# Performance work log

Measured on AMD Instinct MI355X. Metric: run time of the kernel, lower is better.

Reference implementation:

```python
import jax, jax.numpy as jnp
import numpy as np


def setup_inputs() -> dict:
    key = jax.random.key(0)
    ks = jax.random.split(key, 8)
    N, C, T, V = 32, 64, 256, 25
    OUT, INTER, S = 64, 16, 3
    W_SCALE = 0.05  # keep complex softmax exp() well-conditioned
    return {
        "x_real": jax.random.normal(ks[0], (N, C, T, V), jnp.float32),
        "x_imag": jax.random.normal(ks[1], (N, C, T, V), jnp.float32),
        "A": jax.random.uniform(ks[2], (S, V, V), jnp.float32),
        "PA": jax.random.normal(ks[3], (S, V, V), jnp.float32) * 1e-3,
        "Wa": jax.random.normal(ks[4], (S, 2 * INTER, 2 * C), jnp.float32) * W_SCALE,
        "ba": jnp.zeros((S, 2 * INTER), jnp.float32),
        "Wb": jax.random.normal(ks[5], (S, 2 * INTER, 2 * C), jnp.float32) * W_SCALE,
        "bb": jnp.zeros((S, 2 * INTER), jnp.float32),
        "Wd": jax.random.normal(ks[6], (S, 2 * OUT, 2 * C), jnp.float32) * W_SCALE,
        "bd": jnp.zeros((S, 2 * OUT), jnp.float32),
        "bn_weight": jnp.ones((OUT,), jnp.float32),
        "bn_bias": jnp.zeros((OUT,), jnp.float32),
    }


def _cconv1x1(z, W, b):
    # C_Conv2d with k=1: 1x1 conv over concat(real, imag) channels.
    zc = jnp.concatenate([z.real, z.imag], axis=1)          # [N, 2*Cin, T, V]
    o = jnp.einsum("oc,nctv->notv", W, zc) + b[None, :, None, None]
    h = W.shape[0] // 2
    return jax.lax.complex(o[:, :h], o[:, h:])              # [N, Cout, T, V] complex


def _forward(x_real, x_imag, A, PA, Wa, ba, Wb, bb, Wd, bd, bn_weight, bn_bias):
    x = jax.lax.complex(x_real, x_imag)                     # [N, C, T, V]
    N, C, T, V = x.shape
    inter = Wa.shape[1] // 2
    Afull = A + PA                                          # [3, V, V] real
    X2 = x.reshape(N, C * T, V)
    y = None
    for i in range(A.shape[0]):
        A1 = _cconv1x1(x, Wa[i], ba[i])                     # [N, inter, T, V]
        A1 = A1.transpose(0, 3, 1, 2).reshape(N, V, inter * T)
        A2 = _cconv1x1(x, Wb[i], bb[i]).reshape(N, inter * T, V)
        S = jnp.matmul(A1, A2) / (inter * T)                # [N, V, V] complex
        # complex softmax over dim=1 (no max-subtraction, faithful to C_softmax)
        ez = jnp.exp(S)
        S = ez / jnp.sum(ez, axis=1, keepdims=True)
        S = S + Afull[i]
        z = jnp.matmul(X2, S).reshape(N, C, T, V)
        z = _cconv1x1(z, Wd[i], bd[i])                      # [N, OUT, T, V]
        y = z if y is None else y + z
    # C_BatchNorm2d on complex input: complex mean, real variance = E|y-mu|^2
    mu = jnp.mean(y, axis=(0, 2, 3))                        # [OUT] complex
    var = jnp.mean(jnp.abs(y - mu[None, :, None, None]) ** 2, axis=(0, 2, 3))
    yn = (y - mu[None, :, None, None]) / jnp.sqrt(var + 1e-5)[None, :, None, None]
    yn = yn * bn_weight[None, :, None, None] + bn_bias[None, :, None, None]
    yn = yn + x  # down = identity (in_channels == out_channels)
    return jnp.stack([yn.real, yn.imag])                    # [2, N, OUT, T, V] real


def reference(x_real, x_imag, A, PA, Wa, ba, Wb, bb, Wd, bd, bn_weight, bn_bias):
    return _forward(x_real, x_imag, A, PA, Wa, ba, Wb, bb, Wd, bd, bn_weight, bn_bias)
```

## Files before the change

### kernel.cpp

```cpp
#include <hip/hip_runtime.h>
#include <hip/hip_bf16.h>
#include <stdint.h>

#define NN 32
#define CC 64
#define TTOT 256
#define VV 25
#define NS 3
constexpr int TV  = TTOT * VV;
constexpr int CTV = CC * TV;
constexpr size_t PLANE = (size_t)NN * CTV;

typedef unsigned short ushort_t;
using short8 = __attribute__((ext_vector_type(8))) short;
using f32x4  = __attribute__((ext_vector_type(4))) float;

static __device__ __forceinline__ ushort_t f2bf(float f) {
  __hip_bfloat16 h = __float2bfloat16(f);
  return reinterpret_cast<ushort_t&>(h);
}
static __device__ __forceinline__ float bf2f(ushort_t h) {
  union { uint32_t u; float f; } v; v.u = ((uint32_t)h) << 16;
  return v.f;
}
static __device__ __forceinline__ int SWZ(int row, int k) {
  return ((row << 7) + k) ^ ((row & 7) << 3);
}
static __device__ __forceinline__ f32x4 mfma16(short8 a, short8 b, f32x4 c) {
  return __builtin_amdgcn_mfma_f32_16x16x32_bf16(a, b, c, 0, 0, 0);
}
static __device__ __forceinline__ short8 negbf8(short8 x) {
  short8 r;
#pragma unroll
  for (int j = 0; j < 8; ++j) r[j] = x[j] ^ (short)0x8000;
  return r;
}

__global__ __launch_bounds__(256) void k0_wfrag(
    const float* __restrict__ Wd, const float* __restrict__ Wa,
    const float* __restrict__ Wb, ushort_t* __restrict__ wfrag,
    ushort_t* __restrict__ wab)
{
  const int i = blockIdx.x;
  for (int e = threadIdx.x; e < 16384; e += 256) {
    int ot = e >> 11, m = (e >> 9) & 3, l = (e >> 3) & 63, j = e & 7;
    int r  = ot * 16 + (l & 15);
    int c = m * 16 + ((l >> 4) << 2) + (j >> 1), comp = j & 1;
    wfrag[(size_t)i * 16384 + e] = f2bf(Wd[(size_t)i * 16384 + r * 128 + comp * 64 + c]);
  }
  for (int e = threadIdx.x; e < 8192; e += 256) {
    int mt = e >> 11, ks = (e >> 9) & 3, l = (e >> 3) & 63, j = e & 7;
    int r  = mt * 16 + (l & 15);
    int kp = ks * 32 + ((l >> 4) << 3) + j;
    float v = (r < 32) ? Wa[((size_t)i * 32 + r) * 128 + kp]
                       : Wb[((size_t)i * 32 + (r - 32)) * 128 + kp];
    wab[(size_t)i * 8192 + e] = f2bf(v);
  }
}

__global__ __launch_bounds__(256) void k1_spart(
    const float* __restrict__ xr, const float* __restrict__ xi,
    const ushort_t* __restrict__ wab, const float* __restrict__ ba,
    const float* __restrict__ bb, float* __restrict__ Spart)
{
  const int tc = blockIdx.x, n = blockIdx.y;
  const int tid = threadIdx.x, lane = tid & 63, wv = tid >> 6;
  const int r16 = lane & 15, gw = lane >> 4;
  __shared__ alignas(16) ushort_t zc[128 * 128];
  __shared__ alignas(16) ushort_t Ga[32 * 128];
  __shared__ alignas(16) ushort_t Gb[32 * 128];

  for (int e4 = tid; e4 < 128 * 25; e4 += 256) {
    int c = e4 / 25, q = e4 % 25;
    const float* src = (c < 64) ? xr : xi;
    float4 w = *(const float4*)&src[(size_t)n * CTV + (c & 63) * TV + tc * 100 + q * 4];
#pragma unroll
    for (int jj = 0; jj < 4; ++jj) {
      int g = q * 4 + jj, t = g / 25, v = g - t * 25;
      zc[SWZ(t * 32 + v, c)] = f2bf(((const float*)&w)[jj]);
    }
  }
  for (int e = tid; e < 28 * 128; e += 256) {
    int r7 = e >> 7, c = e & 127;
    int t = r7 / 7, vv = 25 + r7 % 7;
    zc[SWZ(t * 32 + vv, c)] = 0;
  }

  const int mu = wv >> 1, nv = wv & 1;

  for (int i = 0; i < NS; ++i) {
    __syncthreads();

    {
      short8 afr[4];
#pragma unroll
      for (int ks = 0; ks < 4; ++ks)
        afr[ks] = *(const short8*)&wab[((((size_t)i * 4 + wv) * 4 + ks) * 64 + lane) * 8];
      float bias[4];
#pragma unroll
      for (int j = 0; j < 4; ++j) {
        int row = wv * 16 + gw * 4 + j;
        bias[j] = (row < 32) ? ba[i * 32 + row] : bb[i * 32 + (row - 32)];
      }
      ushort_t* gbuf = (wv < 2) ? Ga : Gb;
      const int half = (wv & 1) * 64;
      for (int nt = 0; nt < 8; ++nt) {
        f32x4 acc = {0.f, 0.f, 0.f, 0.f};
        const int brow = nt * 16 + r16;
#pragma unroll
        for (int ks = 0; ks < 4; ++ks) {
          short8 bfr = *(const short8*)&zc[SWZ(brow, ks * 32 + gw * 8)];
          acc = mfma16(afr[ks], bfr, acc);
        }
        int pos2 = nt * 16 + r16;
        int t = pos2 >> 5, v = pos2 & 31;
        int k0w = half + t * 16 + gw * 4;
        uint32_t w0 = (uint32_t)f2bf(acc[0] + bias[0]) | ((uint32_t)f2bf(acc[1] + bias[1]) << 16);
        uint32_t w1 = (uint32_t)f2bf(acc[2] + bias[2]) | ((uint32_t)f2bf(acc[3] + bias[3]) << 16);
        uint2 pk; pk.x = w0; pk.y = w1;
        *(uint2*)&gbuf[SWZ(v, k0w)] = pk;
      }
    }
    __syncthreads();

    {
      const int urow = mu * 16 + r16;
      const int vrow = nv * 16 + r16;
      f32x4 Prr = {0.f,0.f,0.f,0.f}, Pii = {0.f,0.f,0.f,0.f};
      f32x4 Pri = {0.f,0.f,0.f,0.f}, Pir = {0.f,0.f,0.f,0.f};
#pragma unroll
      for (int ks = 0; ks < 2; ++ks) {
        int ko = ks * 32 + gw * 8;
        short8 arF = *(const short8*)&Ga[SWZ(urow, ko)];
        short8 aiF = *(const short8*)&Ga[SWZ(urow, 64 + ko)];
        short8 brF = *(const short8*)&Gb[SWZ(vrow, ko)];
        short8 biF = *(const short8*)&Gb[SWZ(vrow, 64 + ko)];
        Prr = mfma16(arF, brF, Prr);
        Pii = mfma16(aiF, biF, Pii);
        Pri = mfma16(arF, biF, Pri);
        Pir = mfma16(aiF, brF, Pir);
      }
#pragma unroll
      for (int j = 0; j < 4; ++j) {
        int u = mu * 16 + gw * 4 + j;
        int v = nv * 16 + r16;
        if (u < VV && v < VV) {
          size_t idx = ((((size_t)i * NN + n) * 64 + tc) * 625 + u * 25 + v) * 2;
          Spart[idx]     = Prr[j] - Pii[j];
          Spart[idx + 1] = Pri[j] + Pir[j];
        }
      }
    }
  }
}

__global__ __launch_bounds__(256) void k2_softmax(
    const float* __restrict__ Spart, const float* __restrict__ Aw,
    const float* __restrict__ PA, ushort_t* __restrict__ sfrag)
{
  const int i = blockIdx.x, n = blockIdx.y, tid = threadIdx.x;
  __shared__ float ez[625 * 2];
  __shared__ float den[25 * 2];
  for (int e = tid; e < 625; e += 256) {
    float sr = 0.f, si = 0.f;
    const float* p = Spart + (((size_t)i * NN + n) * 64 * 625 + e) * 2;
    for (int tcb = 0; tcb < 64; ++tcb) { sr += p[0]; si += p[1]; p += 625 * 2; }
    sr *= (1.f / 4096.f); si *= (1.f / 4096.f);
    float m = expf(sr);
    ez[e * 2] = m * cosf(si);
    ez[e * 2 + 1] = m * sinf(si);
  }
  __syncthreads();
  if (tid < 25) {
    float dr = 0.f, di = 0.f;
    for (int u = 0; u < 25; ++u) { dr += ez[(u * 25 + tid) * 2]; di += ez[(u * 25 + tid) * 2 + 1]; }
    float inv = 1.f / (dr * dr + di * di);
    den[tid * 2] = dr * inv; den[tid * 2 + 1] = -di * inv;
  }
  __syncthreads();
  for (int e = tid; e < 625; e += 256) {
    int v = e % 25;
    float er = ez[e * 2], ei = ez[e * 2 + 1];
    float dr = den[v * 2], di = den[v * 2 + 1];
    float outr = er * dr - ei * di + Aw[i * 625 + e] + PA[i * 625 + e];
    float outi = er * di + ei * dr;
    ez[e * 2] = outr; ez[e * 2 + 1] = outi;
  }
  __syncthreads();
  for (int e = tid; e < 512; e += 256) {
    int l = e & 63, nt = (e >> 6) & 1, m = e >> 7;
    int u0 = (l >> 4) << 3, v = nt * 16 + (l & 15);
    short8 pk;
#pragma unroll
    for (int j = 0; j < 8; ++j) {
      int u = u0 + j;
      float val = 0.f;
      if (u < VV && v < VV) {
        float sr_ = ez[(u * 25 + v) * 2], si_ = ez[(u * 25 + v) * 2 + 1];
        float base = (m < 2) ? sr_ : si_;
        if (m & 1) { float hi = bf2f(f2bf(base)); val = base - hi; }
        else val = base;
      }
      pk[j] = (short)f2bf(val);
    }
    *(short8*)&sfrag[((size_t)(i * NN + n) * 512 + e) * 8] = pk;
  }
}

__global__ __launch_bounds__(512, 2) void k3_y(
    const float* __restrict__ xr, const float* __restrict__ xi,
    const ushort_t* __restrict__ sfrag, const ushort_t* __restrict__ wfrag,
    const float* __restrict__ bd, float* __restrict__ out,
    float* __restrict__ bnpart)
{
  const int tq = blockIdx.x, n = blockIdx.y;
  const int tid = threadIdx.x, lane = tid & 63, wv = tid >> 6;
  const int r16 = lane & 15, gw = lane >> 4;
  __shared__ alignas(16) ushort_t wlds[49152];
  __shared__ float stats[8][128][2];

  {
    ushort_t* xs = wlds;
    for (int e4 = tid; e4 < 128 * 50; e4 += 512) {
      int c = e4 / 50, q = e4 % 50;
      const float* src = (c < 64) ? xr : xi;
      float4 w = *(const float4*)&src[(size_t)n * CTV + (c & 63) * TV + tq * 200 + q * 4];
#pragma unroll
      for (int jj = 0; jj < 4; ++jj) {
        int g = q * 4 + jj, t = g / 25, u = g - t * 25;
        xs[(t >> 2) * 16384 + SWZ(c, (t & 3) * 32 + u)] = f2bf(((const float*)&w)[jj]);
      }
    }
    for (int e = tid; e < 128 * 56; e += 512) {
      int c = e / 56, r = e % 56;
      int t = r / 7, u = 25 + r % 7;
      xs[(t >> 2) * 16384 + SWZ(c, (t & 3) * 32 + u)] = 0;
    }
  }
  __syncthreads();

  const int tl = wv & 3, th = wv >> 2;
  const int kx = tl * 32 + gw * 8;
  short8 axr[4], axi[4];
#pragma unroll
  for (int tile = 0; tile < 4; ++tile) {
    axr[tile] = *(const short8*)&wlds[th * 16384 + SWZ(tile * 16 + r16, kx)];
    axi[tile] = *(const short8*)&wlds[th * 16384 + SWZ(64 + tile * 16 + r16, kx)];
  }
  __syncthreads();

  {
    short8 tmp[12];
#pragma unroll
    for (int q = 0; q < 12; ++q)
      tmp[q] = *(const short8*)&wfrag[(size_t)(q * 512 + tid) * 8];
#pragma unroll
    for (int q = 0; q < 12; ++q)
      *(short8*)&wlds[(size_t)(q * 512 + tid) * 8] = tmp[q];
  }
  __syncthreads();

  f32x4 acc[8][2];
#pragma unroll
  for (int a = 0; a < 8; ++a) { acc[a][0] = {0.f,0.f,0.f,0.f}; acc[a][1] = {0.f,0.f,0.f,0.f}; }

  auto load_sf = [&](int i, short8 sf[4][2]) {
    const ushort_t* sb = sfrag + (size_t)(i * NN + n) * 4096;
#pragma unroll
    for (int m = 0; m < 4; ++m)
#pragma unroll
      for (int nt = 0; nt < 2; ++nt)
        sf[m][nt] = *(const short8*)&sb[((m * 2 + nt) * 64 + lane) * 8];
  };
  auto compute_i = [&](int i, short8 sf[4][2]) {
    short8 sn0[2], sn1[2];
#pragma unroll
    for (int nt = 0; nt < 2; ++nt) { sn0[nt] = negbf8(sf[2][nt]); sn1[nt] = negbf8(sf[3][nt]); }
    short8 bp[4][2];
#pragma unroll
    for (int tile = 0; tile < 4; ++tile) {
#pragma unroll
      for (int nt = 0; nt < 2; ++nt) {
        f32x4 zr = {0.f,0.f,0.f,0.f}, zi = {0.f,0.f,0.f,0.f};
        zr = mfma16(axr[tile], sf[0][nt], zr);
        zr = mfma16(axr[tile], sf[1][nt], zr);
        zr = mfma16(axi[tile], sn0[nt], zr);
        zr = mfma16(axi[tile], sn1[nt], zr);
        zi = mfma16(axr[tile], sf[2][nt], zi);
        zi = mfma16(axr[tile], sf[3][nt], zi);
        zi = mfma16(axi[tile], sf[0][nt], zi);
        zi = mfma16(axi[tile], sf[1][nt], zi);
        short8 pk;
#pragma unroll
        for (int j = 0; j < 4; ++j) {
          pk[2 * j]     = (short)f2bf(zr[j]);
          pk[2 * j + 1] = (short)f2bf(zi[j]);
        }
        bp[tile][nt] = pk;
      }
    }
#pragma unroll
    for (int ot = 0; ot < 8; ++ot) {
#pragma unroll
      for (int m = 0; m < 4; ++m) {
        short8 a = *(const short8*)&wlds[((size_t)i * 16384) + (size_t)((ot * 4 + m) * 64 + lane) * 8];
        acc[ot][0] = mfma16(a, bp[m][0], acc[ot][0]);
        acc[ot][1] = mfma16(a, bp[m][1], acc[ot][1]);
      }
    }
  };

  short8 sfA[4][2], sfB[4][2];
  load_sf(0, sfA);
  load_sf(1, sfB);
  compute_i(0, sfA);
  load_sf(2, sfA);
  compute_i(1, sfB);
  compute_i(2, sfA);

  const int t = tq * 8 + wv;
#pragma unroll
  for (int ot = 0; ot < 8; ++ot) {
#pragma unroll
    for (int j = 0; j < 4; ++j) {
      int row = ot * 16 + gw * 4 + j;
      float bias = bd[row] + bd[128 + row] + bd[256 + row];
      float s = 0.f, q = 0.f;
#pragma unroll
      for (int nt = 0; nt < 2; ++nt) {
        int v = nt * 16 + r16;
        float val = acc[ot][nt][j] + bias;
        if (v < VV) {
          out[(size_t)(row >> 6) * PLANE + (size_t)n * CTV + (row & 63) * TV + t * VV + v] = val;
          s += val; q += val * val;
        }
      }
#pragma unroll
      for (int d = 1; d < 16; d <<= 1) { s += __shfl_xor(s, d); q += __shfl_xor(q, d); }
      if (r16 == 0) { stats[wv][row][0] = s; stats[wv][row][1] = q; }
    }
  }
  __syncthreads();
  if (tid < 128) {
    float s = 0.f, q = 0.f;
#pragma unroll
    for (int w = 0; w < 8; ++w) { s += stats[w][tid][0]; q += stats[w][tid][1]; }
    size_t b = (size_t)n * 32 + tq;
    bnpart[(b * 128 + tid) * 2]     = s;
    bnpart[(b * 128 + tid) * 2 + 1] = q;
  }
}

__global__ __launch_bounds__(256) void k4_stats(
    const float* __restrict__ bnpart, const float* __restrict__ bnw,
    const float* __restrict__ bnb, float* __restrict__ coeff)
{
  const int o = blockIdx.x, tid = threadIdx.x;
  float sr = 0.f, qr = 0.f, si = 0.f, qi = 0.f;
  for (int b = tid; b < 1024; b += 256) {
    const float* p = bnpart + ((size_t)b * 128 + o) * 2;
    sr += p[0]; qr += p[1];
    const float* p2 = bnpart + ((size_t)b * 128 + 64 + o) * 2;
    si += p2[0]; qi += p2[1];
  }
#pragma unroll
  for (int d = 1; d < 64; d <<= 1) {
    sr += __shfl_xor(sr, d); qr += __shfl_xor(qr, d);
    si += __shfl_xor(si, d); qi += __shfl_xor(qi, d);
  }
  __shared__ float red[4][4];
  int lane = tid & 63, wv = tid >> 6;
  if (lane == 0) { red[wv][0] = sr; red[wv][1] = qr; red[wv][2] = si; red[wv][3] = qi; }
  __syncthreads();
  if (tid == 0) {
    sr = red[0][0] + red[1][0] + red[2][0] + red[3][0];
    qr = red[0][1] + red[1][1] + red[2][1] + red[3][1];
    si = red[0][2] + red[1][2] + red[2][2] + red[3][2];
    qi = red[0][3] + red[1][3] + red[2][3] + red[3][3];
    const float invM = 1.f / (float)((size_t)NN * TTOT * VV);
    float mur = sr * invM, mui = si * invM;
    float var = (qr + qi) * invM - mur * mur - mui * mui;
    float inv = rsqrtf(var + 1e-5f);
    coeff[o * 4 + 0] = mur; coeff[o * 4 + 1] = mui;
    coeff[o * 4 + 2] = inv * bnw[o]; coeff[o * 4 + 3] = bnb[o];
  }
}

__global__ __launch_bounds__(256) void k5_norm(
    const float* __restrict__ xr, const float* __restrict__ xi,
    const float* __restrict__ coeff, float* __restrict__ out)
{
  size_t idx0 = ((size_t)blockIdx.x * 256 + threadIdx.x) * 4;
  size_t stride = (size_t)gridDim.x * 256 * 4;
  for (size_t e = idx0; e < PLANE; e += stride) {
    int o = (int)((e / TV) & 63);
    float4 cf = *(const float4*)&coeff[o * 4];
    float4 yr = *(float4*)&out[e];
    float4 yi = *(float4*)&out[PLANE + e];
    float4 vr = *(const float4*)&xr[e];
    float4 vi = *(const float4*)&xi[e];
    yr.x = (yr.x - cf.x) * cf.z + cf.w + vr.x;
    yr.y = (yr.y - cf.x) * cf.z + cf.w + vr.y;
    yr.z = (yr.z - cf.x) * cf.z + cf.w + vr.z;
    yr.w = (yr.w - cf.x) * cf.z + cf.w + vr.w;
    yi.x = (yi.x - cf.y) * cf.z + vi.x;
    yi.y = (yi.y - cf.y) * cf.z + vi.y;
    yi.z = (yi.z - cf.y) * cf.z + vi.z;
    yi.w = (yi.w - cf.y) * cf.z + vi.w;
    *(float4*)&out[e] = yr;
    *(float4*)&out[PLANE + e] = yi;
  }
}

extern "C" void kernel_launch(void* const* d_in, const int* in_sizes, int n_in,
                              void* d_out, int out_size, void* d_ws, size_t ws_size,
                              hipStream_t stream) {
  const float* xr  = (const float*)d_in[0];
  const float* xi  = (const float*)d_in[1];
  const float* Aw  = (const float*)d_in[2];
  const float* PA  = (const float*)d_in[3];
  const float* Wa  = (const float*)d_in[4];
  const float* ba  = (const float*)d_in[5];
  const float* Wb  = (const float*)d_in[6];
  const float* bb  = (const float*)d_in[7];
  const float* Wd  = (const float*)d_in[8];
  const float* bd  = (const float*)d_in[9];
  const float* bnw = (const float*)d_in[10];
  const float* bnb = (const float*)d_in[11];
  float* out = (float*)d_out;
  float* ws = (float*)d_ws;

  float*    Spart  = ws;
  float*    bnpart = ws;
  ushort_t* sfrag  = (ushort_t*)(ws + 7680000);
  ushort_t* wfrag  = (ushort_t*)(ws + 7876608);
  ushort_t* wab    = (ushort_t*)(ws + 7901184);
  float*    coeff  = ws + 7913472;

  k0_wfrag<<<NS, 256, 0, stream>>>(Wd, Wa, Wb, wfrag, wab);
  k1_spart<<<dim3(64, NN), 256, 0, stream>>>(xr, xi, wab, ba, bb, Spart);
  k2_softmax<<<dim3(NS, NN), 256, 0, stream>>>(Spart, Aw, PA, sfrag);
  k3_y<<<dim3(32, NN), 512, 0, stream>>>(xr, xi, sfrag, wfrag, bd, out, bnpart);
  k4_stats<<<64, 256, 0, stream>>>(bnpart, bnw, bnb, coeff);
  k5_norm<<<6400, 256, 0, stream>>>(xr, xi, coeff, out);
}
```

Baseline: 245.2 us.

## Drop bf16 hi/lo split of softmax matrix and batch k1 stage phases

The softmax output S is now stored as a single bf16 value per real and imaginary part instead of a hi/lo bf16 pair. This halves the sfrag fragments and removes half of the MFMAs in k3's X·S step, at the cost of precision in that product. k1 now computes the G projections for all three subsets into separate LDS buffers before one barrier, then does the S partial products. This removes per-iteration syncs but triples the Ga/Gb LDS footprint. k3's launch bounds also drop the min-blocks hint, which changes register and occupancy limits.

Result: no change. 247.1 us (+0.8%).

```diff
diff --git a/kernel.cpp b/kernel.cpp
--- a/kernel.cpp
+++ b/kernel.cpp
@@ -67,8 +67,8 @@
   const int tid = threadIdx.x, lane = tid & 63, wv = tid >> 6;
   const int r16 = lane & 15, gw = lane >> 4;
   __shared__ alignas(16) ushort_t zc[128 * 128];
-  __shared__ alignas(16) ushort_t Ga[32 * 128];
-  __shared__ alignas(16) ushort_t Gb[32 * 128];
+  __shared__ alignas(16) ushort_t Ga[NS][32 * 128];
+  __shared__ alignas(16) ushort_t Gb[NS][32 * 128];
 
   for (int e4 = tid; e4 < 128 * 25; e4 += 256) {
     int c = e4 / 25, q = e4 % 25;
@@ -85,70 +85,68 @@
     int t = r7 / 7, vv = 25 + r7 % 7;
     zc[SWZ(t * 32 + vv, c)] = 0;
   }
+  __syncthreads();
+
+#pragma unroll 1
+  for (int i = 0; i < NS; ++i) {
+    short8 afr[4];
+#pragma unroll
+    for (int ks = 0; ks < 4; ++ks)
+      afr[ks] = *(const short8*)&wab[((((size_t)i * 4 + wv) * 4 + ks) * 64 + lane) * 8];
+    float bias[4];
+#pragma unroll
+    for (int j = 0; j < 4; ++j) {
+      int row = wv * 16 + gw * 4 + j;
+      bias[j] = (row < 32) ? ba[i * 32 + row] : bb[i * 32 + (row - 32)];
+    }
+    ushort_t* gbuf = (wv < 2) ? Ga[i] : Gb[i];
+    const int half = (wv & 1) * 64;
+    for (int nt = 0; nt < 8; ++nt) {
+      f32x4 acc = {0.f, 0.f, 0.f, 0.f};
+      const int brow = nt * 16 + r16;
+#pragma unroll
+      for (int ks = 0; ks < 4; ++ks) {
+        short8 bfr = *(const short8*)&zc[SWZ(brow, ks * 32 + gw * 8)];
+        acc = mfma16(afr[ks], bfr, acc);
+      }
+      int pos2 = nt * 16 + r16;
+      int t = pos2 >> 5, v = pos2 & 31;
+      int k0w = half + t * 16 + gw * 4;
+      uint32_t w0 = (uint32_t)f2bf(acc[0] + bias[0]) | ((uint32_t)f2bf(acc[1] + bias[1]) << 16);
+      uint32_t w1 = (uint32_t)f2bf(acc[2] + bias[2]) | ((uint32_t)f2bf(acc[3] + bias[3]) << 16);
+      uint2 pk; pk.x = w0; pk.y = w1;
+      *(uint2*)&gbuf[SWZ(v, k0w)] = pk;
+    }
+  }
+  __syncthreads();
 
   const int mu = wv >> 1, nv = wv & 1;
-
+  const int urow = mu * 16 + r16;
+  const int vrow = nv * 16 + r16;
+#pragma unroll 1
   for (int i = 0; i < NS; ++i) {
-    __syncthreads();
-
-    {
-      short8 afr[4];
-#pragma unroll
-      for (int ks = 0; ks < 4; ++ks)
-        afr[ks] = *(const short8*)&wab[((((size_t)i * 4 + wv) * 4 + ks) * 64 + lane) * 8];
-      float bias[4];
-#pragma unroll
-      for (int j = 0; j < 4; ++j) {
-        int row = wv * 16 + gw * 4 + j;
-        bias[j] = (row < 32) ? ba[i * 32 + row] : bb[i * 32 + (row - 32)];
-      }
-      ushort_t* gbuf = (wv < 2) ? Ga : Gb;
-      const int half = (wv & 1) * 64;
-      for (int nt = 0; nt < 8; ++nt) {
-        f32x4 acc = {0.f, 0.f, 0.f, 0.f};
-        const int brow = nt * 16 + r16;
-#pragma unroll
-        for (int ks = 0; ks < 4; ++ks) {
-          short8 bfr = *(const short8*)&zc[SWZ(brow, ks * 32 + gw * 8)];
-          acc = mfma16(afr[ks], bfr, acc);
-        }
-        int pos2 = nt * 16 + r16;
-        int t = pos2 >> 5, v = pos2 & 31;
-        int k0w = half + t * 16 + gw * 4;
-        uint32_t w0 = (uint32_t)f2bf(acc[0] + bias[0]) | ((uint32_t)f2bf(acc[1] + bias[1]) << 16);
-        uint32_t w1 = (uint32_t)f2bf(acc[2] + bias[2]) | ((uint32_t)f2bf(acc[3] + bias[3]) << 16);
-        uint2 pk; pk.x = w0; pk.y = w1;
-        *(uint2*)&gbuf[SWZ(v, k0w)] = pk;
-      }
-    }
-    __syncthreads();
-
-    {
-      const int urow = mu * 16 + r16;
-      const int vrow = nv * 16 + r16;
-      f32x4 Prr = {0.f,0.f,0.f,0.f}, Pii = {0.f,0.f,0.f,0.f};
-      f32x4 Pri = {0.f,0.f,0.f,0.f}, Pir = {0.f,0.f,0.f,0.f};
-#pragma unroll
-      for (int ks = 0; ks < 2; ++ks) {
-        int ko = ks * 32 + gw * 8;
-        short8 arF = *(const short8*)&Ga[SWZ(urow, ko)];
-        short8 aiF = *(const short8*)&Ga[SWZ(urow, 64 + ko)];
-        short8 brF = *(const short8*)&Gb[SWZ(vrow, ko)];
-        short8 biF = *(const short8*)&Gb[SWZ(vrow, 64 + ko)];
-        Prr = mfma16(arF, brF, Prr);
-        Pii = mfma16(aiF, biF, Pii);
-        Pri = mfma16(arF, biF, Pri);
-        Pir = mfma16(aiF, brF, Pir);
-      }
-#pragma unroll
-      for (int j = 0; j < 4; ++j) {
-        int u = mu * 16 + gw * 4 + j;
-        int v = nv * 16 + r16;
-        if (u < VV && v < VV) {
-          size_t idx = ((((size_t)i * NN + n) * 64 + tc) * 625 + u * 25 + v) * 2;
-          Spart[idx]     = Prr[j] - Pii[j];
-          Spart[idx + 1] = Pri[j] + Pir[j];
-        }
+    f32x4 Prr = {0.f,0.f,0.f,0.f}, Pii = {0.f,0.f,0.f,0.f};
+    f32x4 Pri = {0.f,0.f,0.f,0.f}, Pir = {0.f,0.f,0.f,0.f};
+#pragma unroll
+    for (int ks = 0; ks < 2; ++ks) {
+      int ko = ks * 32 + gw * 8;
+      short8 arF = *(const short8*)&Ga[i][SWZ(urow, ko)];
+      short8 aiF = *(const short8*)&Ga[i][SWZ(urow, 64 + ko)];
+      short8 brF = *(const short8*)&Gb[i][SWZ(vrow, ko)];
+      short8 biF = *(const short8*)&Gb[i][SWZ(vrow, 64 + ko)];
+      Prr = mfma16(arF, brF, Prr);
+      Pii = mfma16(aiF, biF, Pii);
+      Pri = mfma16(arF, biF, Pri);
+      Pir = mfma16(aiF, brF, Pir);
+    }
+#pragma unroll
+    for (int j = 0; j < 4; ++j) {
+      int u = mu * 16 + gw * 4 + j;
+      int v = nv * 16 + r16;
+      if (u < VV && v < VV) {
+        size_t idx = ((((size_t)i * NN + n) * 64 + tc) * 625 + u * 25 + v) * 2;
+        Spart[idx]     = Prr[j] - Pii[j];
+        Spart[idx + 1] = Pri[j] + Pir[j];
       }
     }
   }
@@ -187,7 +185,7 @@
     ez[e * 2] = outr; ez[e * 2 + 1] = outi;
   }
   __syncthreads();
-  for (int e = tid; e < 512; e += 256) {
+  for (int e = tid; e < 256; e += 256) {
     int l = e & 63, nt = (e >> 6) & 1, m = e >> 7;
     int u0 = (l >> 4) << 3, v = nt * 16 + (l & 15);
     short8 pk;
@@ -195,25 +193,21 @@
     for (int j = 0; j < 8; ++j) {
       int u = u0 + j;
       float val = 0.f;
-      if (u < VV && v < VV) {
-        float sr_ = ez[(u * 25 + v) * 2], si_ = ez[(u * 25 + v) * 2 + 1];
-        float base = (m < 2) ? sr_ : si_;
-        if (m & 1) { float hi = bf2f(f2bf(base)); val = base - hi; }
-        else val = base;
-      }
+      if (u < VV && v < VV)
+        val = (m == 0) ? ez[(u * 25 + v) * 2] : ez[(u * 25 + v) * 2 + 1];
       pk[j] = (short)f2bf(val);
     }
-    *(short8*)&sfrag[((size_t)(i * NN + n) * 512 + e) * 8] = pk;
-  }
-}
-
-__global__ __launch_bounds__(512, 2) void k3_y(
+    *(short8*)&sfrag[((size_t)(i * NN + n) * 256 + e) * 8] = pk;
+  }
+}
+
+__global__ __launch_bounds__(512) void k3_y(
     const float* __restrict__ xr, const float* __restrict__ xi,
     const ushort_t* __restrict__ sfrag, const ushort_t* __restrict__ wfrag,
     const float* __restrict__ bd, float* __restrict__ out,
     float* __restrict__ bnpart)
 {
-  const int tq = blockIdx.x, n = blockIdx.y;
+  const int tq8 = blockIdx.x, n = blockIdx.y;
   const int tid = threadIdx.x, lane = tid & 63, wv = tid >> 6;
   const int r16 = lane & 15, gw = lane >> 4;
   __shared__ alignas(16) ushort_t wlds[49152];
@@ -224,7 +218,7 @@
     for (int e4 = tid; e4 < 128 * 50; e4 += 512) {
       int c = e4 / 50, q = e4 % 50;
       const float* src = (c < 64) ? xr : xi;
-      float4 w = *(const float4*)&src[(size_t)n * CTV + (c & 63) * TV + tq * 200 + q * 4];
+      float4 w = *(const float4*)&src[(size_t)n * CTV + (c & 63) * TV + tq8 * 200 + q * 4];
 #pragma unroll
       for (int jj = 0; jj < 4; ++jj) {
         int g = q * 4 + jj, t = g / 25, u = g - t * 25;
@@ -264,18 +258,18 @@
 #pragma unroll
   for (int a = 0; a < 8; ++a) { acc[a][0] = {0.f,0.f,0.f,0.f}; acc[a][1] = {0.f,0.f,0.f,0.f}; }
 
-  auto load_sf = [&](int i, short8 sf[4][2]) {
-    const ushort_t* sb = sfrag + (size_t)(i * NN + n) * 4096;
-#pragma unroll
-    for (int m = 0; m < 4; ++m)
+  auto load_sf = [&](int i, short8 sf[2][2]) {
+    const ushort_t* sb = sfrag + (size_t)(i * NN + n) * 2048;
+#pragma unroll
+    for (int m = 0; m < 2; ++m)
 #pragma unroll
       for (int nt = 0; nt < 2; ++nt)
         sf[m][nt] = *(const short8*)&sb[((m * 2 + nt) * 64 + lane) * 8];
   };
-  auto compute_i = [&](int i, short8 sf[4][2]) {
-    short8 sn0[2], sn1[2];
-#pragma unroll
-    for (int nt = 0; nt < 2; ++nt) { sn0[nt] = negbf8(sf[2][nt]); sn1[nt] = negbf8(sf[3][nt]); }
+  auto compute_i = [&](int i, short8 sf[2][2]) {
+    short8 snI[2];
+#pragma unroll
+    for (int nt = 0; nt < 2; ++nt) snI[nt] = negbf8(sf[1][nt]);
     short8 bp[4][2];
 #pragma unroll
     for (int tile = 0; tile < 4; ++tile) {
@@ -283,13 +277,9 @@
       for (int nt = 0; nt < 2; ++nt) {
         f32x4 zr = {0.f,0.f,0.f,0.f}, zi = {0.f,0.f,0.f,0.f};
         zr = mfma16(axr[tile], sf[0][nt], zr);
-        zr = mfma16(axr[tile], sf[1][nt], zr);
-        zr = mfma16(axi[tile], sn0[nt], zr);
-        zr = mfma16(axi[tile], sn1[nt], zr);
-        zi = mfma16(axr[tile], sf[2][nt], zi);
-        zi = mfma16(axr[tile], sf[3][nt], zi);
+        zr = mfma16(axi[tile], snI[nt], zr);
+        zi = mfma16(axr[tile], sf[1][nt], zi);
         zi = mfma16(axi[tile], sf[0][nt], zi);
-        zi = mfma16(axi[tile], sf[1][nt], zi);
         short8 pk;
 #pragma unroll
         for (int j = 0; j < 4; ++j) {
@@ -310,7 +300,7 @@
     }
   };
 
-  short8 sfA[4][2], sfB[4][2];
+  short8 sfA[2][2], sfB[2][2];
   load_sf(0, sfA);
   load_sf(1, sfB);
   compute_i(0, sfA);
@@ -318,7 +308,7 @@
   compute_i(1, sfB);
   compute_i(2, sfA);
 
-  const int t = tq * 8 + wv;
+  const int t = tq8 * 8 + wv;
 #pragma unroll
   for (int ot = 0; ot < 8; ++ot) {
 #pragma unroll
@@ -345,7 +335,7 @@
     float s = 0.f, q = 0.f;
 #pragma unroll
     for (int w = 0; w < 8; ++w) { s += stats[w][tid][0]; q += stats[w][tid][1]; }
-    size_t b = (size_t)n * 32 + tq;
+    size_t b = (size_t)n * 32 + tq8;
     bnpart[(b * 128 + tid) * 2]     = s;
     bnpart[(b * 128 + tid) * 2 + 1] = q;
   }
@@ -433,9 +423,9 @@
   float*    Spart  = ws;
   float*    bnpart = ws;
   ushort_t* sfrag  = (ushort_t*)(ws + 7680000);
-  ushort_t* wfrag  = (ushort_t*)(ws + 7876608);
-  ushort_t* wab    = (ushort_t*)(ws + 7901184);
-  float*    coeff  = ws + 7913472;
+  ushort_t* wfrag  = (ushort_t*)(ws + 7778304);
+  ushort_t* wab    = (ushort_t*)(ws + 7802880);
+  float*    coeff  = ws + 7815168;
 
   k0_wfrag<<<NS, 256, 0, stream>>>(Wd, Wa, Wb, wfrag, wab);
   k1_spart<<<dim3(64, NN), 256, 0, stream>>>(xr, xi, wab, ba, bb, Spart);
```
